# Performance work log

Measured on AMD Instinct MI355X. Metric: run time of the kernel, lower is better.

## Reference

```python
import jax, jax.numpy as jnp
import numpy as np

B, DIM_IN, DIM_OUT = 8192, 2048, 512


def setup_inputs() -> dict:
    key = jax.random.key(0)
    k1, k2, k3, k4, k5 = jax.random.split(key, 5)
    s_in = 1.0 / np.sqrt(DIM_IN)
    return {
        "x": jax.random.normal(k1, (B, DIM_IN), dtype=jnp.float32),
        "W_hazard": jax.random.normal(k2, (DIM_OUT, DIM_IN), dtype=jnp.float32) * s_in,
        "b_hazard": jax.random.normal(k3, (DIM_OUT,), dtype=jnp.float32) * s_in,
        "W_base": jax.random.normal(k4, (1, DIM_IN), dtype=jnp.float32) * s_in,
        "b_base": jax.random.normal(k5, (1,), dtype=jnp.float32) * s_in,
    }


def reference(x, W_hazard, b_hazard, W_base, b_base):
    # hazards = ReLU(x @ W_h^T + b_h)  -> [B, T]
    hazards = jax.nn.relu(jnp.einsum("bd,td->bt", x, W_hazard) + b_hazard)
    # Triangular-mask expand+sum is exactly an inclusive prefix sum along T:
    # cum_prob[b, j] = sum_{i <= j} hazards[b, i] + base_hazard[b]
    cum_hazards = jnp.cumsum(hazards, axis=1)
    base_hazard = jnp.einsum("bd,od->bo", x, W_base) + b_base  # [B, 1]
    return cum_hazards + base_hazard
```

## Files before the change

kernel.cpp:

```cpp
#include <hip/hip_runtime.h>
#include <hip/hip_bf16.h>


typedef __attribute__((ext_vector_type(8))) short  short8;
typedef __attribute__((ext_vector_type(4))) short  short4v;
typedef __attribute__((ext_vector_type(4))) float  float4v;
typedef __attribute__((ext_vector_type(4))) float  f32x4;

#define DIN  2048
#define DOUT 512
#define NROW 8192
#define BM   32
#define NPH  (DIN / 64)

static __device__ __forceinline__ unsigned short f2bf(float f) {
  union { float f; unsigned int u; } v; v.f = f;
  unsigned int u = v.u;
  unsigned int r = (u + 0x7FFFu + ((u >> 16) & 1u)) >> 16;
  return (unsigned short)r;
}

static __device__ __forceinline__ void barrier_nd() {
  asm volatile("s_waitcnt lgkmcnt(0)" ::: "memory");
  __builtin_amdgcn_s_barrier();
}

__global__ __launch_bounds__(256) void k_pack(const float* __restrict__ W,
                                              unsigned short* __restrict__ Wp) {
  int t    = blockIdx.x * 256 + threadIdx.x;
  int lane = t & 63;
  int frag = t >> 6;
  int nt   = frag >> 6, ktp = frag & 63;
  int n = nt * 16 + (lane & 15);
  int k = ktp * 32 + (lane >> 4) * 8;
  const float* src = W + (size_t)n * DIN + k;
  float4v a = *(const float4v*)src;
  float4v b = *(const float4v*)(src + 4);
  unsigned short o[8] = { f2bf(a.x), f2bf(a.y), f2bf(a.z), f2bf(a.w),
                          f2bf(b.x), f2bf(b.y), f2bf(b.z), f2bf(b.w) };
  *(short8*)(Wp + (size_t)t * 8) = *(const short8*)o;
}

__global__ __launch_bounds__(1024, 4) void k_main(
    const float* __restrict__ x, const unsigned short* __restrict__ Wp,
    const float* __restrict__ b_h, const float* __restrict__ w_base,
    const float* __restrict__ b_base, float* __restrict__ out) {
  __shared__ unsigned short Asw[2][BM * 64];
  __shared__ float WbL[DIN];
  __shared__ float stripT[BM][16];
  __shared__ float baseL[BM];

  const int tid  = threadIdx.x;
  const int lane = tid & 63;
  const int w    = tid >> 6;
  const int q    = lane >> 4;
  const int lm   = lane & 15;
  const int m0   = blockIdx.x * BM;
  const bool stager = (tid < 512);

  const int sr  = tid >> 4;
  const int seg = tid & 15;
  const int sOff = (sr & 31) * 64 + (((seg >> 1) ^ (sr & 7)) << 3) + (seg & 1) * 4;

  for (int i = tid; i < DIN; i += 1024) WbL[i] = w_base[i];

  f32x4 acc[2][2];
  const f32x4 z4 = {0.f, 0.f, 0.f, 0.f};
#pragma unroll
  for (int mi = 0; mi < 2; ++mi)
#pragma unroll
    for (int ni = 0; ni < 2; ++ni) acc[mi][ni] = z4;

  float4v a0, a1;
  short8  wf0[2][2], wf1[2][2];
  float   basePart = 0.f;

  auto loadA = [&](float4v& A, int kt) {
    if (stager)
      A = *(const float4v*)(x + (size_t)(m0 + sr) * DIN + kt * 64 + seg * 4);
  };
  auto loadB = [&](short8 wf[2][2], int kt) {
#pragma unroll
    for (int ni = 0; ni < 2; ++ni)
#pragma unroll
      for (int h = 0; h < 2; ++h) {
        int frag = (w * 2 + ni) * 64 + (kt * 2 + h);
        wf[ni][h] = *(const short8*)(Wp + ((size_t)frag << 9) + lane * 8);
      }
  };
  auto writeA = [&](unsigned short* As, const float4v& A, int kt) {
    if (stager) {
      unsigned short t4[4] = { f2bf(A.x), f2bf(A.y), f2bf(A.z), f2bf(A.w) };
      *(short4v*)&As[sOff] = *(const short4v*)t4;
      float4v wb = *(const float4v*)&WbL[kt * 64 + seg * 4];
      basePart += A.x * wb.x + A.y * wb.y + A.z * wb.z + A.w * wb.w;
    }
  };
  auto compute = [&](const unsigned short* As, const short8 wf[2][2]) {
#pragma unroll
    for (int h = 0; h < 2; ++h) {
      short8 xf[2];
#pragma unroll
      for (int mi = 0; mi < 2; ++mi) {
        int r = mi * 16 + lm;
        int g = q + 4 * h;
        xf[mi] = *(const short8*)&As[r * 64 + ((g ^ (r & 7)) << 3)];
      }
#pragma unroll
      for (int mi = 0; mi < 2; ++mi)
#pragma unroll
        for (int ni = 0; ni < 2; ++ni)
          acc[mi][ni] = __builtin_amdgcn_mfma_f32_16x16x32_bf16(
              wf[ni][h], xf[mi], acc[mi][ni], 0, 0, 0);
    }
  };

  loadA(a0, 0); loadB(wf0, 0);
  loadA(a1, 1); loadB(wf1, 1);
  barrier_nd();
  writeA(Asw[0], a0, 0);
  barrier_nd();

  for (int kt = 0; kt < NPH; kt += 2) {
    if (kt + 2 < NPH) loadA(a0, kt + 2);
    compute(Asw[0], wf0);
    if (kt + 2 < NPH) loadB(wf0, kt + 2);
    writeA(Asw[1], a1, kt + 1);
    barrier_nd();
    if (kt + 3 < NPH) loadA(a1, kt + 3);
    compute(Asw[1], wf1);
    if (kt + 3 < NPH) loadB(wf1, kt + 3);
    if (kt + 2 < NPH) writeA(Asw[0], a0, kt + 2);
    barrier_nd();
  }

  if (stager) {
    float s = basePart;
    s += __shfl_xor(s, 1); s += __shfl_xor(s, 2);
    s += __shfl_xor(s, 4); s += __shfl_xor(s, 8);
    if (seg == 0) baseL[sr] = s + b_base[0];
  }

  float runp[2][2][4];
  float Eq[2][2];
  float niPre[2][2];
  float Tst[2];
#pragma unroll
  for (int mi = 0; mi < 2; ++mi) {
    float run = 0.f;
#pragma unroll
    for (int ni = 0; ni < 2; ++ni) {
      float4v b4 = *(const float4v*)(b_h + w * 32 + ni * 16 + q * 4);
      f32x4 v = acc[mi][ni];
      float h0 = fmaxf(v.x + b4.x, 0.f);
      float h1 = fmaxf(v.y + b4.y, 0.f);
      float h2 = fmaxf(v.z + b4.z, 0.f);
      float h3 = fmaxf(v.w + b4.w, 0.f);
      runp[mi][ni][0] = h0;
      runp[mi][ni][1] = h0 + h1;
      runp[mi][ni][2] = h0 + h1 + h2;
      runp[mi][ni][3] = h0 + h1 + h2 + h3;
      float S = runp[mi][ni][3];
      float u1 = __shfl_up(S, 16);
      float u2 = __shfl_up(S, 32);
      float u3 = __shfl_up(S, 48);
      Eq[mi][ni] = (q >= 1 ? u1 : 0.f) + (q >= 2 ? u2 : 0.f) + (q >= 3 ? u3 : 0.f);
      float G = S + __shfl_xor(S, 16);
      G += __shfl_xor(G, 32);
      niPre[mi][ni] = run;
      run += G;
    }
    Tst[mi] = run;
  }
  if (q == 0) {
#pragma unroll
    for (int mi = 0; mi < 2; ++mi) stripT[mi * 16 + lm][w] = Tst[mi];
  }
  barrier_nd();

#pragma unroll
  for (int mi = 0; mi < 2; ++mi) {
    const int row = mi * 16 + lm;
    float c = baseL[row];
#pragma unroll
    for (int j4 = 0; j4 < 4; ++j4) {
      float4v s = *(const float4v*)&stripT[row][j4 * 4];
      c += (w > j4 * 4 + 0 ? s.x : 0.f) + (w > j4 * 4 + 1 ? s.y : 0.f) +
           (w > j4 * 4 + 2 ? s.z : 0.f) + (w > j4 * 4 + 3 ? s.w : 0.f);
    }
#pragma unroll
    for (int ni = 0; ni < 2; ++ni) {
      float base = c + niPre[mi][ni] + Eq[mi][ni];
      float4v o = { runp[mi][ni][0] + base, runp[mi][ni][1] + base,
                    runp[mi][ni][2] + base, runp[mi][ni][3] + base };
      *(float4v*)(out + (size_t)(m0 + row) * DOUT + w * 32 + ni * 16 + q * 4) = o;
    }
  }
}

extern "C" void kernel_launch(void* const* d_in, const int* in_sizes, int n_in,
                              void* d_out, int out_size, void* d_ws, size_t ws_size,
                              hipStream_t stream) {
  const float* x   = (const float*)d_in[0];
  const float* Wh  = (const float*)d_in[1];
  const float* bh  = (const float*)d_in[2];
  const float* Wb0 = (const float*)d_in[3];
  const float* bb  = (const float*)d_in[4];
  float* out = (float*)d_out;

  unsigned short* Wp = (unsigned short*)d_ws;

  k_pack<<<dim3((DOUT * DIN) / (256 * 8)), dim3(256), 0, stream>>>(Wh, Wp);
  k_main<<<dim3(NROW / BM), dim3(1024), 0, stream>>>(x, Wp, bh, Wb0, bb, out);
}
```

Before: 41.18 us.

## Stage A in 8-phase chunks with all threads and fewer barriers

The A-tile staging now works on chunks of 8 k-phases (512 columns) instead of one 64-column phase at a time. All 1024 threads load 16 floats each per chunk, where previously only 512 threads loaded 4 each. This cuts the barrier count per k-loop from 64 to 8 and makes the global loads wider per thread. W fragments are no longer register-prefetched a stage ahead; they are loaded inside compute right before use. That may expose global-load latency, and the larger shared buffer (2x32KB) may lower occupancy.

```diff
diff --git a/kernel.cpp b/kernel.cpp
--- a/kernel.cpp
+++ b/kernel.cpp
@@ -12,6 +12,8 @@
 #define NROW 8192
 #define BM   32
 #define NPH  (DIN / 64)
+#define CHP  8
+#define NCH  (NPH / CHP)
 
 static __device__ __forceinline__ unsigned short f2bf(float f) {
   union { float f; unsigned int u; } v; v.f = f;
@@ -45,7 +47,7 @@
     const float* __restrict__ x, const unsigned short* __restrict__ Wp,
     const float* __restrict__ b_h, const float* __restrict__ w_base,
     const float* __restrict__ b_base, float* __restrict__ out) {
-  __shared__ unsigned short Asw[2][BM * 64];
+  __shared__ unsigned short Achk[2][CHP * BM * 64];
   __shared__ float WbL[DIN];
   __shared__ float stripT[BM][16];
   __shared__ float baseL[BM];
@@ -56,11 +58,13 @@
   const int q    = lane >> 4;
   const int lm   = lane & 15;
   const int m0   = blockIdx.x * BM;
-  const bool stager = (tid < 512);
-
-  const int sr  = tid >> 4;
-  const int seg = tid & 15;
-  const int sOff = (sr & 31) * 64 + (((seg >> 1) ^ (sr & 7)) << 3) + (seg & 1) * 4;
+
+  const int sr  = tid >> 5;
+  const int cs  = (tid & 31) * 16;
+  const int sph = cs >> 6;
+  const int sg0 = (cs & 63) >> 3;
+  const int offW0 = sph * 2048 + sr * 64 + (((sg0)     ^ (sr & 7)) << 3);
+  const int offW1 = sph * 2048 + sr * 64 + (((sg0 + 1) ^ (sr & 7)) << 3);
 
   for (int i = tid; i < DIN; i += 1024) WbL[i] = w_base[i];
 
@@ -71,74 +75,75 @@
 #pragma unroll
     for (int ni = 0; ni < 2; ++ni) acc[mi][ni] = z4;
 
-  float4v a0, a1;
-  short8  wf0[2][2], wf1[2][2];
+  float4v st[4];
   float   basePart = 0.f;
 
-  auto loadA = [&](float4v& A, int kt) {
-    if (stager)
-      A = *(const float4v*)(x + (size_t)(m0 + sr) * DIN + kt * 64 + seg * 4);
+  auto stage_load = [&](int c) {
+    const float* p = x + (size_t)(m0 + sr) * DIN + c * (CHP * 64) + cs;
+#pragma unroll
+    for (int i = 0; i < 4; ++i) st[i] = *(const float4v*)(p + i * 4);
   };
-  auto loadB = [&](short8 wf[2][2], int kt) {
-#pragma unroll
-    for (int ni = 0; ni < 2; ++ni)
+  auto stage_write = [&](unsigned short* buf, int c) {
+    unsigned short t16[16];
+#pragma unroll
+    for (int i = 0; i < 4; ++i) {
+      t16[i * 4 + 0] = f2bf(st[i].x); t16[i * 4 + 1] = f2bf(st[i].y);
+      t16[i * 4 + 2] = f2bf(st[i].z); t16[i * 4 + 3] = f2bf(st[i].w);
+      const float4v wb = *(const float4v*)&WbL[c * (CHP * 64) + cs + i * 4];
+      basePart += st[i].x * wb.x + st[i].y * wb.y + st[i].z * wb.z + st[i].w * wb.w;
+    }
+    *(short8*)&buf[offW0] = *(const short8*)&t16[0];
+    *(short8*)&buf[offW1] = *(const short8*)&t16[8];
+  };
+  auto compute = [&](const unsigned short* buf, int c) {
+#pragma unroll
+    for (int ph = 0; ph < CHP; ++ph) {
+      const int pk = c * CHP + ph;
+      short8 bf[2][2];
+#pragma unroll
+      for (int ni = 0; ni < 2; ++ni)
+#pragma unroll
+        for (int h = 0; h < 2; ++h) {
+          int frag = (w * 2 + ni) * 64 + pk * 2 + h;
+          bf[ni][h] = *(const short8*)(Wp + ((size_t)frag << 9) + lane * 8);
+        }
 #pragma unroll
       for (int h = 0; h < 2; ++h) {
-        int frag = (w * 2 + ni) * 64 + (kt * 2 + h);
-        wf[ni][h] = *(const short8*)(Wp + ((size_t)frag << 9) + lane * 8);
+        short8 xf[2];
+#pragma unroll
+        for (int mi = 0; mi < 2; ++mi) {
+          int r = mi * 16 + lm;
+          int g = q + 4 * h;
+          xf[mi] = *(const short8*)&buf[ph * 2048 + r * 64 + ((g ^ (r & 7)) << 3)];
+        }
+#pragma unroll
+        for (int mi = 0; mi < 2; ++mi)
+#pragma unroll
+          for (int ni = 0; ni < 2; ++ni)
+            acc[mi][ni] = __builtin_amdgcn_mfma_f32_16x16x32_bf16(
+                bf[ni][h], xf[mi], acc[mi][ni], 0, 0, 0);
       }
+    }
   };
-  auto writeA = [&](unsigned short* As, const float4v& A, int kt) {
-    if (stager) {
-      unsigned short t4[4] = { f2bf(A.x), f2bf(A.y), f2bf(A.z), f2bf(A.w) };
-      *(short4v*)&As[sOff] = *(const short4v*)t4;
-      float4v wb = *(const float4v*)&WbL[kt * 64 + seg * 4];
-      basePart += A.x * wb.x + A.y * wb.y + A.z * wb.z + A.w * wb.w;
-    }
-  };
-  auto compute = [&](const unsigned short* As, const short8 wf[2][2]) {
-#pragma unroll
-    for (int h = 0; h < 2; ++h) {
-      short8 xf[2];
-#pragma unroll
-      for (int mi = 0; mi < 2; ++mi) {
-        int r = mi * 16 + lm;
-        int g = q + 4 * h;
-        xf[mi] = *(const short8*)&As[r * 64 + ((g ^ (r & 7)) << 3)];
-      }
-#pragma unroll
-      for (int mi = 0; mi < 2; ++mi)
-#pragma unroll
-        for (int ni = 0; ni < 2; ++ni)
-          acc[mi][ni] = __builtin_amdgcn_mfma_f32_16x16x32_bf16(
-              wf[ni][h], xf[mi], acc[mi][ni], 0, 0, 0);
-    }
-  };
-
-  loadA(a0, 0); loadB(wf0, 0);
-  loadA(a1, 1); loadB(wf1, 1);
+
+  stage_load(0);
   barrier_nd();
-  writeA(Asw[0], a0, 0);
+  stage_write(Achk[0], 0);
   barrier_nd();
 
-  for (int kt = 0; kt < NPH; kt += 2) {
-    if (kt + 2 < NPH) loadA(a0, kt + 2);
-    compute(Asw[0], wf0);
-    if (kt + 2 < NPH) loadB(wf0, kt + 2);
-    writeA(Asw[1], a1, kt + 1);
+  for (int c = 0; c < NCH; ++c) {
+    if (c + 1 < NCH) stage_load(c + 1);
+    compute(Achk[c & 1], c);
+    if (c + 1 < NCH) stage_write(Achk[(c + 1) & 1], c + 1);
     barrier_nd();
-    if (kt + 3 < NPH) loadA(a1, kt + 3);
-    compute(Asw[1], wf1);
-    if (kt + 3 < NPH) loadB(wf1, kt + 3);
-    if (kt + 2 < NPH) writeA(Asw[0], a0, kt + 2);
-    barrier_nd();
-  }
-
-  if (stager) {
+  }
+
+  {
     float s = basePart;
-    s += __shfl_xor(s, 1); s += __shfl_xor(s, 2);
-    s += __shfl_xor(s, 4); s += __shfl_xor(s, 8);
-    if (seg == 0) baseL[sr] = s + b_base[0];
+    s += __shfl_xor(s, 1);  s += __shfl_xor(s, 2);
+    s += __shfl_xor(s, 4);  s += __shfl_xor(s, 8);
+    s += __shfl_xor(s, 16);
+    if ((tid & 31) == 0) baseL[sr] = s + b_base[0];
   }
 
   float runp[2][2][4];
```

Measured after the change: 50.41 us. 1.22x slower.
